# Optimization experiments

Hardware: AMD Instinct MI355X
Metric: run time of the kernel (lower is better)

Reference implementation:

```python
import jax, jax.numpy as jnp
import numpy as np

N, E, G = 20000, 320000, 128
H, C, D, ED, L = 4, 64, 256, 64, 4  # heads, per-head dim, node_dim=H*C, edge_dim, layers
NEG = 0.2  # GATv2 leaky_relu slope


def _ln(x, s, b):
    mu = jnp.mean(x, -1, keepdims=True)
    var = jnp.mean((x - mu) ** 2, -1, keepdims=True)
    return (x - mu) * jax.lax.rsqrt(var + 1e-5) * s + b


def _seg_softmax(logits, seg, num):
    m = jax.ops.segment_max(logits, seg, num_segments=num)
    m = jnp.where(jnp.isfinite(m), m, 0.0)
    ex = jnp.exp(logits - m[seg])
    den = jax.ops.segment_sum(ex, seg, num_segments=num)
    return ex / (den[seg] + 1e-16)


def _gatv2(h, e, src, dst, Wl, bl, Wr, br, We, att, bias):
    n = h.shape[0]
    # add_self_loops with fill_value='mean': self-loop edge_attr = mean of incoming edge attrs
    cnt = jax.ops.segment_sum(jnp.ones((dst.shape[0],), h.dtype), dst, num_segments=n)
    loop_e = jax.ops.segment_sum(e, dst, num_segments=n) / jnp.maximum(cnt, 1.0)[:, None]
    ar = jnp.arange(n)
    s = jnp.concatenate([src, ar])
    d = jnp.concatenate([dst, ar])
    ef = jnp.concatenate([e, loop_e], 0)
    xl = (h @ Wl + bl).reshape(n, H, C)  # lin_l -> source messages
    xr = (h @ Wr + br).reshape(n, H, C)  # lin_r -> target
    msg = xl[s] + xr[d] + (ef @ We).reshape(-1, H, C)
    msg = jax.nn.leaky_relu(msg, NEG)
    logits = jnp.einsum('ehc,hc->eh', msg, att)
    alpha = _seg_softmax(logits, d, n)  # softmax over incoming edges per dst
    out = jax.ops.segment_sum(alpha[:, :, None] * xl[s], d, num_segments=n)
    return out.reshape(n, H * C) + bias


def setup_inputs() -> dict:
    key = jax.random.key(0)
    ks = jax.random.split(key, 32)
    f32 = jnp.float32
    inp = {
        'x': jax.random.normal(ks[0], (N, 9), f32),
        'edge_index': jax.random.randint(ks[1], (2, E), 0, N),
        'edge_attr': jax.random.normal(ks[2], (E, 3), f32),
        'batch': jnp.sort(jax.random.randint(ks[3], (N,), 0, G)),
        'atomW': jax.random.normal(ks[4], (9, D), f32) / 3.0,
        'atomB': jnp.zeros((D,), f32),
        'bondW': jax.random.normal(ks[5], (3, ED), f32) / np.sqrt(3.0),
        'bondB': jnp.zeros((ED,), f32),
        'Wl': jax.random.normal(ks[6], (L, D, D), f32) / 16.0,
        'bl': jnp.zeros((L, D), f32),
        'Wr': jax.random.normal(ks[7], (L, D, D), f32) / 16.0,
        'br': jnp.zeros((L, D), f32),
        'We': jax.random.normal(ks[8], (L, ED, D), f32) / 8.0,
        'att': jax.random.normal(ks[9], (L, H, C), f32) / 8.0,
        'bias': jnp.zeros((L, D), f32),
        'ln1s': jnp.ones((L, D), f32),
        'ln1b': jnp.zeros((L, D), f32),
        'eW': jax.random.normal(ks[10], (L, 2 * D + ED, ED), f32) / 24.0,
        'eb': jnp.zeros((L, ED), f32),
        'ln2s': jnp.ones((L, ED), f32),
        'ln2b': jnp.zeros((L, ED), f32),
        'jkW': jax.random.normal(ks[11], (L * D, D), f32) / 32.0,
        'jkb': jnp.zeros((D,), f32),
        'ln3s': jnp.ones((D,), f32),
        'ln3b': jnp.zeros((D,), f32),
        'gW1': jax.random.normal(ks[12], (D, D // 2), f32) / 16.0,
        'gb1': jnp.zeros((D // 2,), f32),
        'gW2': jax.random.normal(ks[13], (D // 2, 1), f32) / 11.3,
        'gb2': jnp.zeros((1,), f32),
        'hW': jax.random.normal(ks[14], (D, 1), f32) / 16.0,
        'hb': jnp.zeros((1,), f32),
    }
    return inp


def reference(x, edge_index, edge_attr, batch, atomW, atomB, bondW, bondB,
              Wl, bl, Wr, br, We, att, bias, ln1s, ln1b, eW, eb, ln2s, ln2b,
              jkW, jkb, ln3s, ln3b, gW1, gb1, gW2, gb2, hW, hb):
    src, dst = edge_index[0], edge_index[1]
    h = x @ atomW + atomB          # atom encoder -> [N, D]
    e = edge_attr @ bondW + bondB  # bond encoder -> [E, ED]
    outs = []
    for l in range(L):
        hn = _gatv2(h, e, src, dst, Wl[l], bl[l], Wr[l], br[l], We[l], att[l], bias[l])
        hn = _ln(jax.nn.silu(hn), ln1s[l], ln1b[l])
        edge_in = jnp.concatenate([hn[src], hn[dst], e], -1)
        e = _ln(jax.nn.silu(edge_in @ eW[l] + eb[l]), ln2s[l], ln2b[l])
        h = hn
        outs.append(h)
    h_jk = jnp.concatenate(outs, -1)  # JK cat -> [N, L*D]
    h = _ln(jax.nn.silu(h_jk @ jkW + jkb), ln3s, ln3b)
    gate = jax.nn.silu(h @ gW1 + gb1) @ gW2 + gb2  # [N, 1]
    gate = _seg_softmax(gate, batch, G)
    h_graph = jax.ops.segment_sum(gate * h, batch, num_segments=G)  # [G, D]
    return h_graph @ hW + hb
```

## Files before the change

kernel.cpp:

```cpp
#include <hip/hip_runtime.h>
#include <hip/hip_bf16.h>

#define N_ 20000
#define E_ 320000
#define G_ 128
#define H_ 4
#define C_ 64
#define D_ 256
#define ED_ 64
#define L_ 4
#define LROW 72

typedef _Float16 f16x8 __attribute__((ext_vector_type(8)));
typedef _Float16 f16x4 __attribute__((ext_vector_type(4)));
typedef float f32x4 __attribute__((ext_vector_type(4)));

__global__ __launch_bounds__(256) void atom_enc(const float* __restrict__ x,
                                                const float* __restrict__ W,
                                                const float* __restrict__ b,
                                                _Float16* __restrict__ h16) {
    int n = blockIdx.x, t = threadIdx.x;
    float acc = b[t];
#pragma unroll
    for (int k = 0; k < 9; ++k) acc += x[n * 9 + k] * W[k * D_ + t];
    h16[(size_t)n * D_ + t] = (_Float16)acc;
}

__global__ __launch_bounds__(256) void bond_enc_perm(const float* __restrict__ ea,
                                                     const float* __restrict__ W,
                                                     const float* __restrict__ b,
                                                     const int* __restrict__ perm,
                                                     _Float16* __restrict__ e16) {
    int idx = blockIdx.x * 256 + threadIdx.x;
    if (idx >= E_ * ED_) return;
    int pos = idx >> 6, j = idx & 63;
    int orig = perm[pos];
    float acc = b[j];
#pragma unroll
    for (int k = 0; k < 3; ++k) acc += ea[orig * 3 + k] * W[k * ED_ + j];
    e16[idx] = (_Float16)acc;
}

__global__ __launch_bounds__(256) void count_kernel(const int* __restrict__ dst,
                                                    int* __restrict__ deg) {
    int e = blockIdx.x * 256 + threadIdx.x;
    if (e >= E_) return;
    atomicAdd(&deg[dst[e]], 1);
}

__global__ __launch_bounds__(1024) void scan_kernel(const int* __restrict__ deg,
                                                    int* __restrict__ row_off) {
    __shared__ int part[1024];
    int t = threadIdx.x;
    const int CH = (N_ + 1023) / 1024;
    int s = 0;
    for (int i = 0; i < CH; ++i) {
        int idx = t * CH + i;
        if (idx < N_) s += deg[idx];
    }
    part[t] = s;
    __syncthreads();
    for (int off = 1; off < 1024; off <<= 1) {
        int v = (t >= off) ? part[t - off] : 0;
        __syncthreads();
        part[t] += v;
        __syncthreads();
    }
    int base = (t == 0) ? 0 : part[t - 1];
    for (int i = 0; i < CH; ++i) {
        int idx = t * CH + i;
        if (idx < N_) { row_off[idx] = base; base += deg[idx]; }
    }
    if (t == 0) row_off[N_] = part[1023];
}

__global__ __launch_bounds__(256) void fill_kernel(const int* __restrict__ src,
                                                   const int* __restrict__ dst,
                                                   const int* __restrict__ row_off,
                                                   int* __restrict__ fill,
                                                   int* __restrict__ perm,
                                                   int* __restrict__ srcp,
                                                   int* __restrict__ dstp) {
    int e = blockIdx.x * 256 + threadIdx.x;
    if (e >= E_) return;
    int d = dst[e];
    int pos = row_off[d] + atomicAdd(&fill[d], 1);
    perm[pos] = e;
    srcp[pos] = src[e];
    dstp[pos] = d;
}

__global__ __launch_bounds__(256) void goff_kernel(const int* __restrict__ batch,
                                                   int* __restrict__ goff) {
    int t = threadIdx.x;
    if (t > G_) return;
    int lo = 0, hi = N_;
    while (lo < hi) { int mid = (lo + hi) >> 1; if (batch[mid] < t) lo = mid + 1; else hi = mid; }
    goff[t] = lo;
}

__global__ __launch_bounds__(256) void pack_wT(const float* __restrict__ W,
                                               _Float16* __restrict__ WT,
                                               int K, int Nn) {
    int idx = blockIdx.x * 256 + threadIdx.x;
    if (idx >= K * Nn) return;
    int n = idx / K, k = idx - n * K;
    WT[idx] = (_Float16)W[(size_t)k * Nn + n];
}

__global__ __launch_bounds__(256) void mfma_gemm(const _Float16* __restrict__ A16,
                                                 const _Float16* __restrict__ BT16,
                                                 const float* __restrict__ bias,
                                                 float* __restrict__ C,
                                                 int M, int K, int Nn, int accum) {
    int t = threadIdx.x;
    int w = t >> 6, l = t & 63;
    int bm = blockIdx.x * 64, bn = blockIdx.y * 64;
    int row0 = bm + w * 16 + (l & 15);
    int arow = row0 < M ? row0 : M - 1;
    int koff = (l >> 4) * 8;
    const _Float16* Ap = A16 + (size_t)arow * K + koff;
    f32x4 acc0 = {}, acc1 = {}, acc2 = {}, acc3 = {};
    for (int ks = 0; ks < K; ks += 32) {
        f16x8 a = *(const f16x8*)(Ap + ks);
        const _Float16* Bp = BT16 + (size_t)(bn + (l & 15)) * K + ks + koff;
        f16x8 b0 = *(const f16x8*)(Bp);
        f16x8 b1 = *(const f16x8*)(Bp + (size_t)16 * K);
        f16x8 b2 = *(const f16x8*)(Bp + (size_t)32 * K);
        f16x8 b3 = *(const f16x8*)(Bp + (size_t)48 * K);
        acc0 = __builtin_amdgcn_mfma_f32_16x16x32_f16(a, b0, acc0, 0, 0, 0);
        acc1 = __builtin_amdgcn_mfma_f32_16x16x32_f16(a, b1, acc1, 0, 0, 0);
        acc2 = __builtin_amdgcn_mfma_f32_16x16x32_f16(a, b2, acc2, 0, 0, 0);
        acc3 = __builtin_amdgcn_mfma_f32_16x16x32_f16(a, b3, acc3, 0, 0, 0);
    }
    f32x4 accs[4] = {acc0, acc1, acc2, acc3};
#pragma unroll
    for (int ct = 0; ct < 4; ++ct) {
        int col = bn + ct * 16 + (l & 15);
#pragma unroll
        for (int r = 0; r < 4; ++r) {
            int row = bm + w * 16 + (l >> 4) * 4 + r;
            if (row < M) {
                float v = accs[ct][r] + (bias ? bias[col] : 0.f);
                if (accum) C[(size_t)row * Nn + col] += v;
                else       C[(size_t)row * Nn + col] = v;
            }
        }
    }
}

__global__ __launch_bounds__(256) void mfma_gemm16(const _Float16* __restrict__ A16,
                                                   const _Float16* __restrict__ BT16,
                                                   const float* __restrict__ bias,
                                                   _Float16* __restrict__ C16,
                                                   int M, int K, int Nn) {
    int t = threadIdx.x;
    int w = t >> 6, l = t & 63;
    int bm = blockIdx.x * 64, bn = blockIdx.y * 64;
    int row0 = bm + w * 16 + (l & 15);
    int arow = row0 < M ? row0 : M - 1;
    int koff = (l >> 4) * 8;
    const _Float16* Ap = A16 + (size_t)arow * K + koff;
    f32x4 acc0 = {}, acc1 = {}, acc2 = {}, acc3 = {};
    for (int ks = 0; ks < K; ks += 32) {
        f16x8 a = *(const f16x8*)(Ap + ks);
        const _Float16* Bp = BT16 + (size_t)(bn + (l & 15)) * K + ks + koff;
        f16x8 b0 = *(const f16x8*)(Bp);
        f16x8 b1 = *(const f16x8*)(Bp + (size_t)16 * K);
        f16x8 b2 = *(const f16x8*)(Bp + (size_t)32 * K);
        f16x8 b3 = *(const f16x8*)(Bp + (size_t)48 * K);
        acc0 = __builtin_amdgcn_mfma_f32_16x16x32_f16(a, b0, acc0, 0, 0, 0);
        acc1 = __builtin_amdgcn_mfma_f32_16x16x32_f16(a, b1, acc1, 0, 0, 0);
        acc2 = __builtin_amdgcn_mfma_f32_16x16x32_f16(a, b2, acc2, 0, 0, 0);
        acc3 = __builtin_amdgcn_mfma_f32_16x16x32_f16(a, b3, acc3, 0, 0, 0);
    }
    f32x4 accs[4] = {acc0, acc1, acc2, acc3};
#pragma unroll
    for (int ct = 0; ct < 4; ++ct) {
        int col = bn + ct * 16 + (l & 15);
        float bv = bias ? bias[col] : 0.f;
#pragma unroll
        for (int r = 0; r < 4; ++r) {
            int row = bm + w * 16 + (l >> 4) * 4 + r;
            if (row < M) C16[(size_t)row * Nn + col] = (_Float16)(accs[ct][r] + bv);
        }
    }
}

__global__ __launch_bounds__(256) void edge_logits_mfma(const _Float16* __restrict__ e16,
                                                        const _Float16* __restrict__ weT16,
                                                        const _Float16* __restrict__ xlr16,
                                                        const int* __restrict__ srcp,
                                                        const int* __restrict__ dstp,
                                                        const float* __restrict__ att,
                                                        float* __restrict__ exlog) {
    __shared__ _Float16 es[64 * LROW];
    __shared__ int ssrc[64], sdst[64];
    int t = threadIdx.x;
    int w = t >> 6, l = t & 63;
    int base = blockIdx.x * 64;
    {
        int row = t >> 2, seg = t & 3;
        const _Float16* gp = e16 + (size_t)(base + row) * ED_ + seg * 16;
        uint4 v0 = *(const uint4*)(gp);
        uint4 v1 = *(const uint4*)(gp + 8);
        _Float16* lp = es + row * LROW + seg * 16;
        *(uint4*)(lp) = v0;
        *(uint4*)(lp + 8) = v1;
    }
    if (t < 64) { ssrc[t] = srcp[base + t]; sdst[t] = dstp[base + t]; }
    __syncthreads();
    int koff = (l >> 4) * 8;
    int cgrp = l & 15;
    f16x8 bf[4][2];
#pragma unroll
    for (int nt = 0; nt < 4; ++nt) {
        const _Float16* bp = weT16 + (size_t)(w * 64 + nt * 16 + cgrp) * 64 + koff;
        bf[nt][0] = *(const f16x8*)(bp);
        bf[nt][1] = *(const f16x8*)(bp + 32);
    }
    f32x4 acc[4][4] = {};
#pragma unroll
    for (int mt = 0; mt < 4; ++mt) {
        f16x8 a0 = *(const f16x8*)(es + (mt * 16 + cgrp) * LROW + koff);
        f16x8 a1 = *(const f16x8*)(es + (mt * 16 + cgrp) * LROW + 32 + koff);
#pragma unroll
        for (int nt = 0; nt < 4; ++nt) {
            acc[mt][nt] = __builtin_amdgcn_mfma_f32_16x16x32_f16(a0, bf[nt][0], acc[mt][nt], 0, 0, 0);
            acc[mt][nt] = __builtin_amdgcn_mfma_f32_16x16x32_f16(a1, bf[nt][1], acc[mt][nt], 0, 0, 0);
        }
    }
    float av[4];
#pragma unroll
    for (int nt = 0; nt < 4; ++nt) av[nt] = att[w * 64 + nt * 16 + cgrp];
#pragma unroll
    for (int mt = 0; mt < 4; ++mt) {
#pragma unroll
        for (int r = 0; r < 4; ++r) {
            int eidx = mt * 16 + (l >> 4) * 4 + r;
            int s = ssrc[eidx], d = sdst[eidx];
            float v = 0.f;
#pragma unroll
            for (int nt = 0; nt < 4; ++nt) {
                int col = w * 64 + nt * 16 + cgrp;
                float m = (float)xlr16[(size_t)s * 512 + col]
                        + (float)xlr16[(size_t)d * 512 + 256 + col]
                        + acc[mt][nt][r];
                m = (m > 0.f) ? m : 0.2f * m;
                v += m * av[nt];
            }
            v += __shfl_xor(v, 1); v += __shfl_xor(v, 2);
            v += __shfl_xor(v, 4); v += __shfl_xor(v, 8);
            if (cgrp == 0) exlog[(size_t)(base + eidx) * H_ + w] = expf(v);
        }
    }
}

__global__ __launch_bounds__(256) void esum_kernel(const _Float16* __restrict__ e16,
                                                   const int* __restrict__ row_off,
                                                   _Float16* __restrict__ esum16) {
    int d = blockIdx.x * 4 + (threadIdx.x >> 6);
    int lane = threadIdx.x & 63;
    if (d >= N_) return;
    int beg = row_off[d], end = row_off[d + 1];
    float s = 0.f;
    for (int i = beg; i < end; ++i) s += (float)e16[(size_t)i * ED_ + lane];
    esum16[(size_t)d * ED_ + lane] = (_Float16)s;
}

__global__ __launch_bounds__(256) void gat_agg4(const _Float16* __restrict__ xlr16,
                                                const _Float16* __restrict__ loopW16,
                                                const int* __restrict__ row_off,
                                                const int* __restrict__ srcp,
                                                const float* __restrict__ exlog,
                                                const float* __restrict__ att,
                                                const float* __restrict__ bias,
                                                const float* __restrict__ gs,
                                                const float* __restrict__ gb,
                                                _Float16* __restrict__ hn16) {
    int t = threadIdx.x;
    int w = t >> 6, lane = t & 63;
    int d = blockIdx.x * 4 + w;
    if (d >= N_) return;
    int beg = row_off[d], end = row_off[d + 1];
    int deg = end - beg;
    int hh = lane >> 4;
    float4 av = *(const float4*)&att[lane * 4];
    f16x4 xld_h = *(const f16x4*)&xlr16[(size_t)d * 512 + lane * 4];
    f16x4 xrd_h = *(const f16x4*)&xlr16[(size_t)d * 512 + 256 + lane * 4];
    float xld[4], xrd[4];
#pragma unroll
    for (int j = 0; j < 4; ++j) { xld[j] = (float)xld_h[j]; xrd[j] = (float)xrd_h[j]; }
    float den = 0.f;
    float out[4] = {0.f, 0.f, 0.f, 0.f};
    int i = beg;
    for (; i + 4 <= end; i += 4) {
        int s0 = srcp[i], s1 = srcp[i + 1], s2 = srcp[i + 2], s3 = srcp[i + 3];
        float ex0 = exlog[(size_t)i * H_ + hh];
        float ex1 = exlog[(size_t)(i + 1) * H_ + hh];
        float ex2 = exlog[(size_t)(i + 2) * H_ + hh];
        float ex3 = exlog[(size_t)(i + 3) * H_ + hh];
        f16x4 x0 = *(const f16x4*)&xlr16[(size_t)s0 * 512 + lane * 4];
        f16x4 x1 = *(const f16x4*)&xlr16[(size_t)s1 * 512 + lane * 4];
        f16x4 x2 = *(const f16x4*)&xlr16[(size_t)s2 * 512 + lane * 4];
        f16x4 x3 = *(const f16x4*)&xlr16[(size_t)s3 * 512 + lane * 4];
        den += (ex0 + ex1) + (ex2 + ex3);
#pragma unroll
        for (int j = 0; j < 4; ++j)
            out[j] += ex0 * (float)x0[j] + ex1 * (float)x1[j] +
                      ex2 * (float)x2[j] + ex3 * (float)x3[j];
    }
    for (; i < end; ++i) {
        int s0 = srcp[i];
        float ex0 = exlog[(size_t)i * H_ + hh];
        f16x4 x0 = *(const f16x4*)&xlr16[(size_t)s0 * 512 + lane * 4];
        den += ex0;
#pragma unroll
        for (int j = 0; j < 4; ++j) out[j] += ex0 * (float)x0[j];
    }
    f16x4 lw4 = *(const f16x4*)&loopW16[(size_t)d * D_ + lane * 4];
    float idg = (deg > 0) ? 1.f / (float)deg : 0.f;
    {
        float v = 0.f;
        float avv[4] = {av.x, av.y, av.z, av.w};
#pragma unroll
        for (int j = 0; j < 4; ++j) {
            float m = xld[j] + xrd[j] + (float)lw4[j] * idg;
            m = (m > 0.f) ? m : 0.2f * m;
            v += m * avv[j];
        }
        v += __shfl_xor(v, 1); v += __shfl_xor(v, 2);
        v += __shfl_xor(v, 4); v += __shfl_xor(v, 8);
        float eself = expf(v);
        den += eself;
#pragma unroll
        for (int j = 0; j < 4; ++j) out[j] += eself * xld[j];
    }
    float inv = 1.f / (den + 1e-16f);
    float4 b4 = *(const float4*)&bias[lane * 4];
    float bv[4] = {b4.x, b4.y, b4.z, b4.w};
    float v4[4], s = 0.f;
#pragma unroll
    for (int j = 0; j < 4; ++j) {
        float v = out[j] * inv + bv[j];
        v = v / (1.f + expf(-v));
        v4[j] = v;
        s += v;
    }
#pragma unroll
    for (int o = 32; o; o >>= 1) s += __shfl_xor(s, o);
    float mu = s * (1.f / 256.f);
    float q = 0.f;
#pragma unroll
    for (int j = 0; j < 4; ++j) { float dv = v4[j] - mu; q += dv * dv; }
#pragma unroll
    for (int o = 32; o; o >>= 1) q += __shfl_xor(q, o);
    float rs = rsqrtf(q * (1.f / 256.f) + 1e-5f);
    float4 g4 = *(const float4*)&gs[lane * 4];
    float4 gb4 = *(const float4*)&gb[lane * 4];
    f16x4 o4;
    float gsv[4] = {g4.x, g4.y, g4.z, g4.w};
    float gbv[4] = {gb4.x, gb4.y, gb4.z, gb4.w};
#pragma unroll
    for (int j = 0; j < 4; ++j) o4[j] = (_Float16)((v4[j] - mu) * rs * gsv[j] + gbv[j]);
    *(f16x4*)&hn16[(size_t)d * D_ + lane * 4] = o4;
}

__global__ __launch_bounds__(256) void edge_mlp_mfma(_Float16* __restrict__ e16,
                                                     const _Float16* __restrict__ ew3T16,
                                                     const _Float16* __restrict__ hsd16,
                                                     const int* __restrict__ srcp,
                                                     const int* __restrict__ dstp,
                                                     const float* __restrict__ eb,
                                                     const float* __restrict__ gs,
                                                     const float* __restrict__ gb) {
    int t = threadIdx.x;
    int w = t >> 6, l = t & 63;
    int bm = blockIdx.x * 64;
    int arow = bm + w * 16 + (l & 15);
    int koff = (l >> 4) * 8;
    const _Float16* Ap = e16 + (size_t)arow * ED_ + koff;
    f16x8 a0 = *(const f16x8*)(Ap);
    f16x8 a1 = *(const f16x8*)(Ap + 32);
    f32x4 acc[4];
#pragma unroll
    for (int nt = 0; nt < 4; ++nt) {
        const _Float16* bp = ew3T16 + (size_t)(nt * 16 + (l & 15)) * 64 + koff;
        f16x8 b0 = *(const f16x8*)(bp);
        f16x8 b1 = *(const f16x8*)(bp + 32);
        f32x4 z = {};
        z = __builtin_amdgcn_mfma_f32_16x16x32_f16(a0, b0, z, 0, 0, 0);
        z = __builtin_amdgcn_mfma_f32_16x16x32_f16(a1, b1, z, 0, 0, 0);
        acc[nt] = z;
    }
    int rbase = bm + w * 16 + (l >> 4) * 4;
#pragma unroll
    for (int r = 0; r < 4; ++r) {
        int row = rbase + r;
        int s = srcp[row], d = dstp[row];
        float v4[4], ss = 0.f;
#pragma unroll
        for (int nt = 0; nt < 4; ++nt) {
            int col = nt * 16 + (l & 15);
            float vv = acc[nt][r] + (float)hsd16[(size_t)s * 128 + col]
                     + (float)hsd16[(size_t)d * 128 + 64 + col] + eb[col];
            vv = vv / (1.f + expf(-vv));
            v4[nt] = vv;
            ss += vv;
        }
        ss += __shfl_xor(ss, 1); ss += __shfl_xor(ss, 2);
        ss += __shfl_xor(ss, 4); ss += __shfl_xor(ss, 8);
        float mu = ss * (1.f / 64.f);
        float q = 0.f;
#pragma unroll
        for (int nt = 0; nt < 4; ++nt) { float dv = v4[nt] - mu; q += dv * dv; }
        q += __shfl_xor(q, 1); q += __shfl_xor(q, 2);
        q += __shfl_xor(q, 4); q += __shfl_xor(q, 8);
        float rs = rsqrtf(q * (1.f / 64.f) + 1e-5f);
#pragma unroll
        for (int nt = 0; nt < 4; ++nt) {
            int col = nt * 16 + (l & 15);
            e16[(size_t)row * ED_ + col] = (_Float16)((v4[nt] - mu) * rs * gs[col] + gb[col]);
        }
    }
}

__global__ __launch_bounds__(256) void node_silu_ln(const float* __restrict__ inp,
                                                    const float* __restrict__ gs,
                                                    const float* __restrict__ gb,
                                                    float* __restrict__ outp,
                                                    _Float16* __restrict__ outp16) {
    int n = blockIdx.x, t = threadIdx.x;
    float v = inp[(size_t)n * D_ + t];
    v = v / (1.f + expf(-v));
    __shared__ float red[4];
    float s = v;
#pragma unroll
    for (int o = 32; o; o >>= 1) s += __shfl_xor(s, o);
    if ((t & 63) == 0) red[t >> 6] = s;
    __syncthreads();
    float mu = (red[0] + red[1] + red[2] + red[3]) * (1.f / 256.f);
    __syncthreads();
    float dv = v - mu;
    float q = dv * dv;
#pragma unroll
    for (int o = 32; o; o >>= 1) q += __shfl_xor(q, o);
    if ((t & 63) == 0) red[t >> 6] = q;
    __syncthreads();
    float var = (red[0] + red[1] + red[2] + red[3]) * (1.f / 256.f);
    float r = dv * rsqrtf(var + 1e-5f) * gs[t] + gb[t];
    outp[(size_t)n * D_ + t] = r;
    outp16[(size_t)n * D_ + t] = (_Float16)r;
}

__global__ __launch_bounds__(256) void gate_lite(const float* __restrict__ hid,
                                                 const float* __restrict__ gW2,
                                                 const float* __restrict__ gb2,
                                                 float* __restrict__ g) {
    int t = threadIdx.x;
    int w = t >> 6, lane = t & 63;
    int n = blockIdx.x * 4 + w;
    if (n >= N_) return;
    float2 h2 = *(const float2*)&hid[(size_t)n * 128 + lane * 2];
    float w0 = gW2[lane * 2], w1 = gW2[lane * 2 + 1];
    float s0 = h2.x / (1.f + expf(-h2.x));
    float s1 = h2.y / (1.f + expf(-h2.y));
    float v = s0 * w0 + s1 * w1;
#pragma unroll
    for (int o = 32; o; o >>= 1) v += __shfl_xor(v, o);
    if (lane == 0) g[n] = v + gb2[0];
}

__global__ __launch_bounds__(256) void graphpool(const float* __restrict__ hfin,
                                                 const float* __restrict__ g,
                                                 const int* __restrict__ goff,
                                                 const float* __restrict__ hW,
                                                 const float* __restrict__ hb,
                                                 float* __restrict__ out) {
    int b = blockIdx.x, t = threadIdx.x;
    int w = t >> 6, lane = t & 63;
    int beg = goff[b], end = goff[b + 1];
    __shared__ float red[4];
    __shared__ float wls[256];
    float den = 0.f;
    for (int n = beg + t; n < end; n += 256) den += expf(g[n]);
#pragma unroll
    for (int o = 32; o; o >>= 1) den += __shfl_xor(den, o);
    if (lane == 0) red[w] = den;
    __syncthreads();
    float dtot = red[0] + red[1] + red[2] + red[3];
    float inv = 1.f / (dtot + 1e-16f);
    float acc = 0.f;
    for (int c0 = beg; c0 < end; c0 += 256) {
        int nn = min(256, end - c0);
        __syncthreads();
        if (t < nn) wls[t] = expf(g[c0 + t]) * inv;
        __syncthreads();
        for (int j = 0; j < nn; ++j)
            acc += wls[j] * hfin[(size_t)(c0 + j) * D_ + t];
    }
    float v = acc * hW[t];
#pragma unroll
    for (int o = 32; o; o >>= 1) v += __shfl_xor(v, o);
    __syncthreads();
    if (lane == 0) red[w] = v;
    __syncthreads();
    if (t == 0) out[b] = red[0] + red[1] + red[2] + red[3] + hb[0];
}

extern "C" void kernel_launch(void* const* d_in, const int* in_sizes, int n_in,
                              void* d_out, int out_size, void* d_ws, size_t ws_size,
                              hipStream_t stream) {
    const float* x     = (const float*)d_in[0];
    const int*   eidx  = (const int*)d_in[1];
    const float* eattr = (const float*)d_in[2];
    const int*   batch = (const int*)d_in[3];
    const float* atomW = (const float*)d_in[4];
    const float* atomB = (const float*)d_in[5];
    const float* bondW = (const float*)d_in[6];
    const float* bondB = (const float*)d_in[7];
    const float* Wl    = (const float*)d_in[8];
    const float* bl    = (const float*)d_in[9];
    const float* Wr    = (const float*)d_in[10];
    const float* br    = (const float*)d_in[11];
    const float* We    = (const float*)d_in[12];
    const float* att   = (const float*)d_in[13];
    const float* bias  = (const float*)d_in[14];
    const float* ln1s  = (const float*)d_in[15];
    const float* ln1b  = (const float*)d_in[16];
    const float* eW    = (const float*)d_in[17];
    const float* eb    = (const float*)d_in[18];
    const float* ln2s  = (const float*)d_in[19];
    const float* ln2b  = (const float*)d_in[20];
    const float* jkW   = (const float*)d_in[21];
    const float* jkb   = (const float*)d_in[22];
    const float* ln3s  = (const float*)d_in[23];
    const float* ln3b  = (const float*)d_in[24];
    const float* gW1   = (const float*)d_in[25];
    const float* gb1   = (const float*)d_in[26];
    const float* gW2   = (const float*)d_in[27];
    const float* gb2   = (const float*)d_in[28];
    const float* hW    = (const float*)d_in[29];
    const float* hb    = (const float*)d_in[30];

    const int* src = eidx;
    const int* dst = eidx + E_;

    char* wp = (char*)d_ws;
    auto take = [&](size_t bytes) {
        char* p = wp;
        wp += (bytes + 255) & ~(size_t)255;
        return (void*)p;
    };
    _Float16*  e16     = (_Float16*)take((size_t)E_ * ED_ * 2);
    _Float16*  xlr16   = (_Float16*)take((size_t)N_ * 512 * 2);
    float*     jkacc   = (float*)take((size_t)N_ * D_ * 4);
    _Float16*  loopW16 = (_Float16*)take((size_t)N_ * D_ * 2);
    float*     hfin    = (float*)take((size_t)N_ * D_ * 4);
    _Float16*  hfin16  = (_Float16*)take((size_t)N_ * D_ * 2);
    float*     hid     = (float*)take((size_t)N_ * 128 * 4);
    _Float16*  h16A    = (_Float16*)take((size_t)N_ * D_ * 2);
    _Float16*  h16B    = (_Float16*)take((size_t)N_ * D_ * 2);
    _Float16*  hsd16   = (_Float16*)take((size_t)N_ * 128 * 2);
    float*     exlog   = (float*)take((size_t)E_ * H_ * 4);
    _Float16*  esum16  = (_Float16*)take((size_t)N_ * ED_ * 2);
    _Float16*  wlrT16  = (_Float16*)take((size_t)L_ * 512 * D_ * 2);
    _Float16*  weT16   = (_Float16*)take((size_t)L_ * ED_ * D_ * 2);
    _Float16*  ewsdT16 = (_Float16*)take((size_t)L_ * 128 * D_ * 2);
    _Float16*  ew3T16  = (_Float16*)take((size_t)L_ * ED_ * ED_ * 2);
    _Float16*  jkwT16  = (_Float16*)take((size_t)L_ * D_ * D_ * 2);
    _Float16*  g1T16   = (_Float16*)take((size_t)D_ * 128 * 2);
    float*     blr     = (float*)take((size_t)L_ * 512 * 4);
    int*   deg_i   = (int*)take((size_t)N_ * 4);
    int*   fill    = (int*)take((size_t)N_ * 4);
    int*   row_off = (int*)take((size_t)(N_ + 1) * 4);
    int*   goff    = (int*)take((size_t)(G_ + 1) * 4);
    int*   perm    = (int*)take((size_t)E_ * 4);
    int*   srcp    = (int*)take((size_t)E_ * 4);
    int*   dstp    = (int*)take((size_t)E_ * 4);
    float* g       = (float*)take((size_t)N_ * 4);

    auto pack = [&](const float* W, _Float16* WT, int K, int Nn) {
        pack_wT<<<(K * Nn + 255) / 256, 256, 0, stream>>>(W, WT, K, Nn);
    };
    for (int l = 0; l < L_; ++l) {
        pack(Wl + (size_t)l * D_ * D_, wlrT16 + (size_t)l * 512 * D_, D_, D_);
        pack(Wr + (size_t)l * D_ * D_, wlrT16 + (size_t)l * 512 * D_ + (size_t)D_ * D_, D_, D_);
        pack(We + (size_t)l * ED_ * D_, weT16 + (size_t)l * ED_ * D_, ED_, D_);
        const float* eW_l = eW + (size_t)l * (2 * D_ + ED_) * ED_;
        pack(eW_l,                        ewsdT16 + (size_t)l * 128 * D_, D_, ED_);
        pack(eW_l + (size_t)D_ * ED_,     ewsdT16 + (size_t)l * 128 * D_ + (size_t)ED_ * D_, D_, ED_);
        pack(eW_l + (size_t)2 * D_ * ED_, ew3T16 + (size_t)l * ED_ * ED_, ED_, ED_);
        pack(jkW + (size_t)l * D_ * D_,   jkwT16 + (size_t)l * D_ * D_, D_, D_);
        hipMemcpyAsync(blr + (size_t)l * 512,       bl + (size_t)l * D_, D_ * 4,
                       hipMemcpyDeviceToDevice, stream);
        hipMemcpyAsync(blr + (size_t)l * 512 + D_,  br + (size_t)l * D_, D_ * 4,
                       hipMemcpyDeviceToDevice, stream);
    }
    pack(gW1, g1T16, D_, 128);

    hipMemsetAsync(deg_i, 0, (size_t)N_ * 4, stream);
    hipMemsetAsync(fill, 0, (size_t)N_ * 4, stream);
    count_kernel<<<(E_ + 255) / 256, 256, 0, stream>>>(dst, deg_i);
    scan_kernel<<<1, 1024, 0, stream>>>(deg_i, row_off);
    fill_kernel<<<(E_ + 255) / 256, 256, 0, stream>>>(src, dst, row_off, fill,
                                                      perm, srcp, dstp);
    goff_kernel<<<1, 256, 0, stream>>>(batch, goff);

    atom_enc<<<N_, 256, 0, stream>>>(x, atomW, atomB, h16A);
    bond_enc_perm<<<(E_ * ED_ + 255) / 256, 256, 0, stream>>>(eattr, bondW, bondB,
                                                              perm, e16);

    const int MB = (N_ + 63) / 64;
    const _Float16* h16_prev = h16A;
    for (int l = 0; l < L_; ++l) {
        const float* att_l = att + (size_t)l * H_ * C_;
        const float* bias_l = bias + (size_t)l * D_;
        const float* ln1s_l = ln1s + (size_t)l * D_;
        const float* ln1b_l = ln1b + (size_t)l * D_;
        const float* eb_l = eb + (size_t)l * ED_;
        const float* ln2s_l = ln2s + (size_t)l * ED_;
        const float* ln2b_l = ln2b + (size_t)l * ED_;
        const _Float16* weT_l = weT16 + (size_t)l * ED_ * D_;
        _Float16* hn16_l = (l & 1) ? h16A : h16B;

        mfma_gemm16<<<dim3(MB, 8), 256, 0, stream>>>(h16_prev,
                                                     wlrT16 + (size_t)l * 512 * D_,
                                                     blr + (size_t)l * 512,
                                                     xlr16, N_, D_, 512);

        esum_kernel<<<(N_ + 3) / 4, 256, 0, stream>>>(e16, row_off, esum16);
        mfma_gemm16<<<dim3(MB, 4), 256, 0, stream>>>(esum16, weT_l, nullptr,
                                                     loopW16, N_, ED_, D_);

        edge_logits_mfma<<<E_ / 64, 256, 0, stream>>>(e16, weT_l, xlr16,
                                                      srcp, dstp, att_l, exlog);

        gat_agg4<<<(N_ + 3) / 4, 256, 0, stream>>>(xlr16, loopW16, row_off, srcp,
                                                   exlog, att_l, bias_l,
                                                   ln1s_l, ln1b_l, hn16_l);

        mfma_gemm16<<<dim3(MB, 2), 256, 0, stream>>>(hn16_l,
                                                     ewsdT16 + (size_t)l * 128 * D_,
                                                     nullptr, hsd16, N_, D_, 128);
        edge_mlp_mfma<<<E_ / 64, 256, 0, stream>>>(e16, ew3T16 + (size_t)l * ED_ * ED_,
                                                   hsd16, srcp, dstp,
                                                   eb_l, ln2s_l, ln2b_l);

        mfma_gemm<<<dim3(MB, 4), 256, 0, stream>>>(hn16_l, jkwT16 + (size_t)l * D_ * D_,
                                                   (l == 0) ? jkb : nullptr,
                                                   jkacc, N_, D_, D_, (l == 0) ? 0 : 1);

        h16_prev = hn16_l;
    }

    node_silu_ln<<<N_, 256, 0, stream>>>(jkacc, ln3s, ln3b, hfin, hfin16);

    mfma_gemm<<<dim3(MB, 2), 256, 0, stream>>>(hfin16, g1T16, gb1, hid, N_, D_, 128, 0);
    gate_lite<<<(N_ + 3) / 4, 256, 0, stream>>>(hid, gW2, gb2, g);
    graphpool<<<G_, 256, 0, stream>>>(hfin, g, goff, hW, hb, (float*)d_out);
}
```

Before: 1.439 ms.

## Permute edge weight columns for vectorized gathers and drop LDS staging in edge logits

```diff
diff --git a/kernel.cpp b/kernel.cpp
--- a/kernel.cpp
+++ b/kernel.cpp
@@ -9,7 +9,6 @@
 #define D_ 256
 #define ED_ 64
 #define L_ 4
-#define LROW 72
 
 typedef _Float16 f16x8 __attribute__((ext_vector_type(8)));
 typedef _Float16 f16x4 __attribute__((ext_vector_type(4)));
@@ -106,6 +105,17 @@
     if (idx >= K * Nn) return;
     int n = idx / K, k = idx - n * K;
     WT[idx] = (_Float16)W[(size_t)k * Nn + n];
+}
+
+__global__ __launch_bounds__(256) void pack_wT_perm(const float* __restrict__ W,
+                                                    _Float16* __restrict__ WTp) {
+    int idx = blockIdx.x * 256 + threadIdx.x;
+    if (idx >= 64 * 256) return;
+    int q = idx >> 6, k = idx & 63;
+    int hw = q >> 6, qq = q & 63;
+    int nt = qq >> 4, cgrp = qq & 15;
+    int n = hw * 64 + cgrp * 4 + nt;
+    WTp[idx] = (_Float16)W[(size_t)k * 256 + n];
 }
 
 __global__ __launch_bounds__(256) void mfma_gemm(const _Float16* __restrict__ A16,
@@ -188,66 +198,54 @@
 }
 
 __global__ __launch_bounds__(256) void edge_logits_mfma(const _Float16* __restrict__ e16,
-                                                        const _Float16* __restrict__ weT16,
+                                                        const _Float16* __restrict__ weTp16,
                                                         const _Float16* __restrict__ xlr16,
                                                         const int* __restrict__ srcp,
                                                         const int* __restrict__ dstp,
                                                         const float* __restrict__ att,
                                                         float* __restrict__ exlog) {
-    __shared__ _Float16 es[64 * LROW];
     __shared__ int ssrc[64], sdst[64];
     int t = threadIdx.x;
     int w = t >> 6, l = t & 63;
     int base = blockIdx.x * 64;
-    {
-        int row = t >> 2, seg = t & 3;
-        const _Float16* gp = e16 + (size_t)(base + row) * ED_ + seg * 16;
-        uint4 v0 = *(const uint4*)(gp);
-        uint4 v1 = *(const uint4*)(gp + 8);
-        _Float16* lp = es + row * LROW + seg * 16;
-        *(uint4*)(lp) = v0;
-        *(uint4*)(lp + 8) = v1;
-    }
     if (t < 64) { ssrc[t] = srcp[base + t]; sdst[t] = dstp[base + t]; }
-    __syncthreads();
     int koff = (l >> 4) * 8;
     int cgrp = l & 15;
     f16x8 bf[4][2];
 #pragma unroll
     for (int nt = 0; nt < 4; ++nt) {
-        const _Float16* bp = weT16 + (size_t)(w * 64 + nt * 16 + cgrp) * 64 + koff;
+        const _Float16* bp = weTp16 + (size_t)(w * 64 + nt * 16 + cgrp) * 64 + koff;
         bf[nt][0] = *(const f16x8*)(bp);
         bf[nt][1] = *(const f16x8*)(bp + 32);
     }
-    f32x4 acc[4][4] = {};
+    float4 av4 = *(const float4*)&att[w * 64 + cgrp * 4];
+    float av[4] = {av4.x, av4.y, av4.z, av4.w};
+    __syncthreads();
 #pragma unroll
     for (int mt = 0; mt < 4; ++mt) {
-        f16x8 a0 = *(const f16x8*)(es + (mt * 16 + cgrp) * LROW + koff);
-        f16x8 a1 = *(const f16x8*)(es + (mt * 16 + cgrp) * LROW + 32 + koff);
+        const _Float16* ap = e16 + (size_t)(base + mt * 16 + cgrp) * ED_ + koff;
+        f16x8 a0 = *(const f16x8*)(ap);
+        f16x8 a1 = *(const f16x8*)(ap + 32);
+        f32x4 acc[4];
 #pragma unroll
         for (int nt = 0; nt < 4; ++nt) {
-            acc[mt][nt] = __builtin_amdgcn_mfma_f32_16x16x32_f16(a0, bf[nt][0], acc[mt][nt], 0, 0, 0);
-            acc[mt][nt] = __builtin_amdgcn_mfma_f32_16x16x32_f16(a1, bf[nt][1], acc[mt][nt], 0, 0, 0);
+            f32x4 z = {};
+            z = __builtin_amdgcn_mfma_f32_16x16x32_f16(a0, bf[nt][0], z, 0, 0, 0);
+            z = __builtin_amdgcn_mfma_f32_16x16x32_f16(a1, bf[nt][1], z, 0, 0, 0);
+            acc[nt] = z;
         }
-    }
-    float av[4];
-#pragma unroll
-    for (int nt = 0; nt < 4; ++nt) av[nt] = att[w * 64 + nt * 16 + cgrp];
-#pragma unroll
-    for (int mt = 0; mt < 4; ++mt) {
 #pragma unroll
         for (int r = 0; r < 4; ++r) {
             int eidx = mt * 16 + (l >> 4) * 4 + r;
             int s = ssrc[eidx], d = sdst[eidx];
+            f16x4 xlv = *(const f16x4*)&xlr16[(size_t)s * 512 + w * 64 + cgrp * 4];
+            f16x4 xrv = *(const f16x4*)&xlr16[(size_t)d * 512 + 256 + w * 64 + cgrp * 4];
             float v = 0.f;
 #pragma unroll
-            for (int nt = 0; nt < 4; ++nt) {
-                int col = w * 64 + nt * 16 + cgrp;
-                float m = (float)xlr16[(size_t)s * 512 + col]
-                        + (float)xlr16[(size_t)d * 512 + 256 + col]
-                        + acc[mt][nt][r];
+            for (int j = 0; j < 4; ++j) {
+                float m = (float)xlv[j] + (float)xrv[j] + acc[j][r];
                 m = (m > 0.f) ? m : 0.2f * m;
-                v += m * av[nt];
+                v += m * av[j];
             }
             v += __shfl_xor(v, 1); v += __shfl_xor(v, 2);
             v += __shfl_xor(v, 4); v += __shfl_xor(v, 8);
@@ -566,6 +564,7 @@
     _Float16*  esum16  = (_Float16*)take((size_t)N_ * ED_ * 2);
     _Float16*  wlrT16  = (_Float16*)take((size_t)L_ * 512 * D_ * 2);
     _Float16*  weT16   = (_Float16*)take((size_t)L_ * ED_ * D_ * 2);
+    _Float16*  weTp16  = (_Float16*)take((size_t)L_ * ED_ * D_ * 2);
     _Float16*  ewsdT16 = (_Float16*)take((size_t)L_ * 128 * D_ * 2);
     _Float16*  ew3T16  = (_Float16*)take((size_t)L_ * ED_ * ED_ * 2);
     _Float16*  jkwT16  = (_Float16*)take((size_t)L_ * D_ * D_ * 2);
@@ -587,6 +586,8 @@
         pack(Wl + (size_t)l * D_ * D_, wlrT16 + (size_t)l * 512 * D_, D_, D_);
         pack(Wr + (size_t)l * D_ * D_, wlrT16 + (size_t)l * 512 * D_ + (size_t)D_ * D_, D_, D_);
         pack(We + (size_t)l * ED_ * D_, weT16 + (size_t)l * ED_ * D_, ED_, D_);
+        pack_wT_perm<<<(64 * 256 + 255) / 256, 256, 0, stream>>>(
+            We + (size_t)l * ED_ * D_, weTp16 + (size_t)l * ED_ * D_);
         const float* eW_l = eW + (size_t)l * (2 * D_ + ED_) * ED_;
         pack(eW_l,                        ewsdT16 + (size_t)l * 128 * D_, D_, ED_);
         pack(eW_l + (size_t)D_ * ED_,     ewsdT16 + (size_t)l * 128 * D_ + (size_t)ED_ * D_, D_, ED_);
@@ -633,8 +634,9 @@
         mfma_gemm16<<<dim3(MB, 4), 256, 0, stream>>>(esum16, weT_l, nullptr,
                                                      loopW16, N_, ED_, D_);
 
-        edge_logits_mfma<<<E_ / 64, 256, 0, stream>>>(e16, weT_l, xlr16,
-                                                      srcp, dstp, att_l, exlog);
+        edge_logits_mfma<<<E_ / 64, 256, 0, stream>>>(e16,
+                                                      weTp16 + (size_t)l * ED_ * D_,
+                                                      xlr16, srcp, dstp, att_l, exlog);
 
         gat_agg4<<<(N_ + 3) / 4, 256, 0, stream>>>(xlr16, loopW16, row_off, srcp,
                                                    exlog, att_l, bias_l,
```

Result: faster. 1.380 ms (-4.1%).
